# Optimization experiments

Hardware: AMD Instinct MI355X
Metric: run time of the kernel (lower is better)

The kernel has to match this reference:

```python
import jax, jax.numpy as jnp
import numpy as np


def setup_inputs() -> dict:
    key = jax.random.key(0)
    k1, k2, k3, k4 = jax.random.split(key, 4)
    B, T, D, H = 4, 4096, 1024, 64
    x = jax.random.normal(k1, (B, T, D), dtype=jnp.float32)
    # nn.Linear(n_embd, head_size, bias=False): store as [D, H] so x @ W matches
    scale = 1.0 / np.sqrt(D)
    Wq = jax.random.normal(k2, (D, H), dtype=jnp.float32) * scale
    Wk = jax.random.normal(k3, (D, H), dtype=jnp.float32) * scale
    Wv = jax.random.normal(k4, (D, H), dtype=jnp.float32) * scale
    return {"x": x, "Wq": Wq, "Wk": Wk, "Wv": Wv}


def reference(x, Wq, Wk, Wv):
    B, T, D = x.shape
    q = jnp.einsum('btd,dh->bth', x, Wq)
    k = jnp.einsum('btd,dh->bth', x, Wk)
    v = jnp.einsum('btd,dh->bth', x, Wv)
    # NOTE: original scales by D**-0.5 where D = n_embd (input dim), not head_size
    scores = jnp.einsum('bth,bsh->bts', q, k) * (D ** -0.5)  # [B,T,T]
    causal = jnp.tril(jnp.ones((T, T), dtype=bool))
    scores = jnp.where(causal, scores, -jnp.inf)
    attn = jax.nn.softmax(scores, axis=-1)
    return jnp.einsum('bts,bsh->bth', attn, v)
```

## Files before the change

kernel.cpp:

```cpp
#include <hip/hip_runtime.h>
#include <hip/hip_bf16.h>
#include <math.h>

typedef __attribute__((ext_vector_type(8))) short bf16x8;
typedef __attribute__((ext_vector_type(4))) float f32x4;
typedef __attribute__((ext_vector_type(16))) float f32x16;
typedef __attribute__((ext_vector_type(2))) unsigned uint2v;

#define MFMA16(A, B, C) __builtin_amdgcn_mfma_f32_16x16x32_bf16(A, B, C, 0, 0, 0)
#define MFMA32(A, B, C) __builtin_amdgcn_mfma_f32_32x32x16_bf16(A, B, C, 0, 0, 0)
#define LOG2E 1.44269504f
#define MB 5.7707801f

__device__ __forceinline__ short f2bf(float f) {
  union { __hip_bfloat16 b; short s; } v;
  v.b = __float2bfloat16(f);
  return v.s;
}

__device__ __forceinline__ float bf2f(short s) {
  union { unsigned u; float f; } v;
  v.u = ((unsigned)(unsigned short)s) << 16;
  return v.f;
}

__device__ __forceinline__ bf16x8 cvt8(float4 a, float4 b) {
  bf16x8 r;
  r[0] = f2bf(a.x); r[1] = f2bf(a.y); r[2] = f2bf(a.z); r[3] = f2bf(a.w);
  r[4] = f2bf(b.x); r[5] = f2bf(b.y); r[6] = f2bf(b.z); r[7] = f2bf(b.w);
  return r;
}

__device__ __forceinline__ unsigned cvt_pk(float lo, float hi) {
  unsigned r;
  asm("v_cvt_pk_bf16_f32 %0, %1, %2" : "=v"(r) : "v"(lo), "v"(hi));
  return r;
}

__device__ __forceinline__ void glds16(const void* g, void* l) {
  __builtin_amdgcn_global_load_lds(
      (const __attribute__((address_space(1))) unsigned int*)g,
      (__attribute__((address_space(3))) unsigned int*)l, 16, 0, 0);
}

__device__ __forceinline__ float xhalf_sum(float x) {
  uint2v r = __builtin_amdgcn_permlane32_swap(__float_as_uint(x), __float_as_uint(x),
                                              false, false);
  return __uint_as_float(r[0]) + __uint_as_float(r[1]);
}

__global__ __launch_bounds__(256) void prep_w(const float* __restrict__ Wq,
                                              const float* __restrict__ Wk,
                                              const float* __restrict__ Wv,
                                              short* __restrict__ Wt) {
  __shared__ float ls[64][65];
  const int wsel = blockIdx.x >> 4;
  const int dt = blockIdx.x & 15;
  const float* W = (wsel == 0) ? Wq : ((wsel == 1) ? Wk : Wv);
  const float scale = (wsel == 0) ? (0.03125f * LOG2E) : 1.0f;
  const int d0 = dt * 64;
  const int rr = threadIdx.x >> 4;
  const int cc = threadIdx.x & 15;
#pragma unroll
  for (int p = 0; p < 4; ++p) {
    int d = rr + p * 16;
    float4 v = *(const float4*)(W + (size_t)(d0 + d) * 64 + cc * 4);
    ls[d][cc * 4 + 0] = v.x; ls[d][cc * 4 + 1] = v.y;
    ls[d][cc * 4 + 2] = v.z; ls[d][cc * 4 + 3] = v.w;
  }
  __syncthreads();
#pragma unroll
  for (int p = 0; p < 4; ++p) {
    int h = rr + p * 16;
    short4 o;
    o.x = f2bf(ls[cc * 4 + 0][h] * scale);
    o.y = f2bf(ls[cc * 4 + 1][h] * scale);
    o.z = f2bf(ls[cc * 4 + 2][h] * scale);
    o.w = f2bf(ls[cc * 4 + 3][h] * scale);
    *(short4*)(Wt + (size_t)(wsel * 64 + h) * 1024 + d0 + cc * 4) = o;
  }
}

__global__ __launch_bounds__(256, 2) void qkv_kernel(const float* __restrict__ x,
                                                     const short* __restrict__ Wt,
                                                     short* __restrict__ qo,
                                                     short* __restrict__ ko,
                                                     short* __restrict__ vT) {
  __shared__ __align__(16) char pool[65536];
  const int tid = threadIdx.x;
  const int wave = tid >> 6, lane = tid & 63;
  const int lr = lane & 15, lq = lane >> 4;
  const int m0 = blockIdx.x * 32;

  f32x4 acc[2][3];
#pragma unroll
  for (int mi = 0; mi < 2; ++mi)
#pragma unroll
    for (int j = 0; j < 3; ++j) acc[mi][j] = f32x4{0.f, 0.f, 0.f, 0.f};

  const int xrow0 = wave * 4 + (lane >> 4);
  const int col16 = lane & 15;
  const float* xg[2];
#pragma unroll
  for (int r = 0; r < 2; ++r) {
    int row = xrow0 + r * 16;
    xg[r] = x + (size_t)(m0 + row) * 1024 + ((col16 ^ (row & 7)) << 2);
  }
  const int wswz = ((lane & 7) ^ (lane >> 3)) << 3;
  const short* wg[6];
#pragma unroll
  for (int r = 0; r < 6; ++r) {
    int n = wave * 8 + (lane >> 3) + r * 32;
    wg[r] = Wt + (size_t)n * 1024 + wswz;
  }
  const int xdst = wave * 1024;
  const int wdst = 8192 + wave * 1024;

#define STAGEQ(c, t)                                                        \
  {                                                                         \
    char* pb = pool + (c) * 32768;                                          \
    glds16(xg[0] + (t) * 64, pb + xdst);                                    \
    glds16(xg[1] + (t) * 64, pb + xdst + 4096);                             \
    _Pragma("unroll") for (int r = 0; r < 6; ++r)                           \
        glds16(wg[r] + (t) * 64, pb + wdst + r * 4096);                     \
  }

  STAGEQ(0, 0)
  __syncthreads();

  int cur = 0;
  for (int t = 0; t < 16; ++t) {
    if (t < 15) STAGEQ(cur ^ 1, t + 1)
    const char* xb = pool + cur * 32768;
    const char* wb = xb + 8192;
#pragma unroll
    for (int kc = 0; kc < 2; ++kc) {
      bf16x8 bfg[3];
#pragma unroll
      for (int j = 0; j < 3; ++j) {
        int n = (wave * 3 + j) * 16 + lr;
        int unit = kc * 4 + lq;
        bfg[j] = *(const bf16x8*)(wb + n * 128 + ((unit ^ (n & 7)) << 4));
      }
#pragma unroll
      for (int mi = 0; mi < 2; ++mi) {
        int row = mi * 16 + lr;
        int p = kc * 4 + lq;
        const char* xr = xb + row * 256;
        float4 a0 = *(const float4*)(xr + (((2 * p) ^ (row & 7)) << 4));
        float4 a1 = *(const float4*)(xr + (((2 * p + 1) ^ (row & 7)) << 4));
        bf16x8 af = cvt8(a0, a1);
#pragma unroll
        for (int j = 0; j < 3; ++j) acc[mi][j] = MFMA16(af, bfg[j], acc[mi][j]);
      }
    }
    __syncthreads();
    cur ^= 1;
  }
#undef STAGEQ

  short* els = (short*)pool;
#pragma unroll
  for (int j = 0; j < 3; ++j) {
    int nt = wave * 3 + j;
#pragma unroll
    for (int mi = 0; mi < 2; ++mi) {
      if (nt < 8) {
#pragma unroll
        for (int r = 0; r < 4; ++r) {
          int mloc = mi * 16 + lq * 4 + r;
          els[mloc * 136 + nt * 16 + lr] = f2bf(acc[mi][j][r]);
        }
      } else {
        int m = m0 + mi * 16 + lq * 4;
        short4 h;
        h.x = f2bf(acc[mi][j][0]); h.y = f2bf(acc[mi][j][1]);
        h.z = f2bf(acc[mi][j][2]); h.w = f2bf(acc[mi][j][3]);
        *(short4*)(vT + ((m >> 12) << 18) + ((nt * 16 + lr - 128) << 12) +
                   (m & 4095)) = h;
      }
    }
  }
  __syncthreads();
  {
    const int m = tid >> 3, nq = tid & 7;
    bf16x8 vq = *(const bf16x8*)(els + m * 136 + nq * 8);
    bf16x8 vk = *(const bf16x8*)(els + m * 136 + 64 + nq * 8);
    *(bf16x8*)(qo + (size_t)(m0 + m) * 64 + nq * 8) = vq;
    *(bf16x8*)(ko + (size_t)(m0 + m) * 64 + nq * 8) = vk;
  }
}

__global__ __launch_bounds__(256) void attn_partial(const short* __restrict__ qbuf,
                                                    const short* __restrict__ kbuf,
                                                    const short* __restrict__ vbuf,
                                                    short* __restrict__ Op,
                                                    float* __restrict__ lp) {
  __shared__ __align__(16) char kv_lds[2][16384];
  const int id = blockIdx.x;
  const int b = id & 3;
  const int u = id >> 2;
  int qt = 0, base = 0;
  while (u >= base + (qt >> 1) + 1) { base += (qt >> 1) + 1; ++qt; }
  const int seg = u - base;
  const int kv_lo = seg << 8;
  const int kv_hi = (seg == (qt >> 1)) ? (qt * 128 + 128) : ((seg + 1) << 8);

  const int tid = threadIdx.x;
  const int wv = tid >> 6, lane = tid & 63;
  const int l31 = lane & 31, hi = lane >> 5;
  const int qr0 = qt * 128 + wv * 32;
  const int qglob = qr0 + l31;

  const short* qb = qbuf + ((size_t)b << 18);
  const short* kb = kbuf + ((size_t)b << 18);
  const short* vb = vbuf + ((size_t)b << 18);

  bf16x8 bq[4];
#pragma unroll
  for (int c = 0; c < 4; ++c)
    bq[c] = *(const bf16x8*)(qb + (size_t)(qr0 + l31) * 64 + c * 16 + hi * 8);

  const int sr = (wv << 4) + (lane >> 3);
  const int swz_s = ((lane & 7) ^ (lane >> 3)) << 3;
  const short* ksrc = kb + (size_t)sr * 64 + swz_s;
  const short* vsrc = vb + (size_t)sr * 4096 + swz_s;
  const int kdst = (wv * 2) * 1024;
  const int vdst = 8192 + (wv * 2) * 1024;

#define STAGE(c, KV0)                                                       \
  {                                                                         \
    char* base_ = kv_lds[c];                                                \
    glds16(ksrc + (size_t)(KV0) * 64, base_ + kdst);                        \
    glds16(ksrc + (size_t)((KV0) + 8) * 64, base_ + kdst + 1024);           \
    glds16(vsrc + (KV0), base_ + vdst);                                     \
    glds16(vsrc + 8 * 4096 + (KV0), base_ + vdst + 1024);                   \
  }

  f32x16 o0, o1;
#pragma unroll
  for (int r = 0; r < 16; ++r) { o0[r] = 0.f; o1[r] = 0.f; }
  float lrow = 0.f;

  union U8 { unsigned u[4]; bf16x8 v; };
  const int swz_r = (l31 & 7);

  STAGE(0, kv_lo)
  __syncthreads();

  int cur = 0;
  for (int kv0 = kv_lo; kv0 < kv_hi; kv0 += 64) {
    if (kv0 + 64 < kv_hi) STAGE(cur ^ 1, kv0 + 64)

    if (kv0 <= qr0 + 31) {
      const int kv1 = kv0 + 32;
      const char* kl = kv_lds[cur];
      const char* vl = kv_lds[cur] + 8192;
      bf16x8 ka[4], kc[4], va[8];
#pragma unroll
      for (int c = 0; c < 4; ++c) {
        ka[c] = *(const bf16x8*)(kl + l31 * 128 + (((c * 2 + hi) ^ swz_r) << 4));
        kc[c] = *(const bf16x8*)(kl + (32 + l31) * 128 + (((c * 2 + hi) ^ swz_r) << 4));
      }
#pragma unroll
      for (int h = 0; h < 2; ++h)
#pragma unroll
        for (int p = 0; p < 4; ++p)
          va[h * 4 + p] = *(const bf16x8*)(vl + (32 * h + l31) * 128 +
                                           (((2 * p + hi) ^ swz_r) << 4));

      f32x16 s0, s1;
#pragma unroll
      for (int r = 0; r < 16; ++r) { s0[r] = 0.f; s1[r] = 0.f; }
#pragma unroll
      for (int c = 0; c < 4; ++c) {
        s0 = MFMA32(ka[c], bq[c], s0);
        s1 = MFMA32(kc[c], bq[c], s1);
      }

      if (kv0 + 31 > qr0) {
#pragma unroll
        for (int r = 0; r < 16; ++r)
          if (kv0 + (r & 3) + 8 * (r >> 2) + 4 * hi > qglob) s0[r] = -1e30f;
      }
      if (kv1 + 31 > qr0) {
#pragma unroll
        for (int r = 0; r < 16; ++r)
          if (kv1 + (r & 3) + 8 * (r >> 2) + 4 * hi > qglob) s1[r] = -1e30f;
      }

      float p0[16], p1[16];
#pragma unroll
      for (int r = 0; r < 16; ++r) {
        p0[r] = exp2f(s0[r] - MB);
        p1[r] = exp2f(s1[r] - MB);
      }
      float a8[8];
#pragma unroll
      for (int r = 0; r < 8; ++r) a8[r] = (p0[r] + p0[r + 8]) + (p1[r] + p1[r + 8]);
      float s4 = ((a8[0] + a8[4]) + (a8[1] + a8[5])) +
                 ((a8[2] + a8[6]) + (a8[3] + a8[7]));
      lrow += xhalf_sum(s4);

#define MAKE_FRAGS(P, UA, UB)                                                  \
      {                                                                        \
        unsigned c0 = cvt_pk(P[0], P[1]), c1 = cvt_pk(P[2], P[3]);             \
        unsigned c2 = cvt_pk(P[4], P[5]), c3 = cvt_pk(P[6], P[7]);             \
        unsigned c4 = cvt_pk(P[8], P[9]), c5 = cvt_pk(P[10], P[11]);           \
        unsigned c6 = cvt_pk(P[12], P[13]), c7 = cvt_pk(P[14], P[15]);         \
        uint2v rA = __builtin_amdgcn_permlane32_swap(c0, c2, false, false);    \
        uint2v rB = __builtin_amdgcn_permlane32_swap(c1, c3, false, false);    \
        uint2v rC = __builtin_amdgcn_permlane32_swap(c4, c6, false, false);    \
        uint2v rD = __builtin_amdgcn_permlane32_swap(c5, c7, false, false);    \
        UA.u[0] = rA[0]; UA.u[2] = rA[1];                                      \
        UA.u[1] = rB[0]; UA.u[3] = rB[1];                                      \
        UB.u[0] = rC[0]; UB.u[2] = rC[1];                                      \
        UB.u[1] = rD[0]; UB.u[3] = rD[1];                                      \
      }
      U8 pa00, pa01, pa10, pa11;
      MAKE_FRAGS(p0, pa00, pa01)
      MAKE_FRAGS(p1, pa10, pa11)
#undef MAKE_FRAGS

      o0 = MFMA32(va[0], pa00.v, o0);
      o0 = MFMA32(va[1], pa01.v, o0);
      o0 = MFMA32(va[2], pa10.v, o0);
      o0 = MFMA32(va[3], pa11.v, o0);
      o1 = MFMA32(va[4], pa00.v, o1);
      o1 = MFMA32(va[5], pa01.v, o1);
      o1 = MFMA32(va[6], pa10.v, o1);
      o1 = MFMA32(va[7], pa11.v, o1);
    }

    __syncthreads();
    cur ^= 1;
  }
#undef STAGE

  const int pid = b * 272 + u;
  short* Ob = Op + (size_t)pid * 8192;
#pragma unroll
  for (int r = 0; r < 16; ++r) {
    int hd = (r & 3) + 8 * (r >> 2) + 4 * hi;
    Ob[hd * 128 + wv * 32 + l31] = f2bf(o0[r]);
    Ob[(32 + hd) * 128 + wv * 32 + l31] = f2bf(o1[r]);
  }
  if (hi == 0) lp[pid * 128 + wv * 32 + l31] = lrow;
}

__global__ __launch_bounds__(256) void attn_combine(const short* __restrict__ Op,
                                                    const float* __restrict__ lp,
                                                    float* __restrict__ out) {
  __shared__ float ls[32][128];
  const int qt = blockIdx.x;
  const int b = blockIdx.y;
  const int zh = blockIdx.z;
  const int m = qt >> 1, e = qt & 1;
  const int nseg = m + 1;
  const int base = b * 272 + qt + m * (m - 1) + e * m;

  const int qc = threadIdx.x & 127, hh = threadIdx.x >> 7;
  float lsum = 0.f;
  for (int s = 0; s < nseg; ++s) lsum += lp[(base + s) * 128 + qc];
  const float inv = 1.0f / lsum;

  float osum[16];
#pragma unroll
  for (int i = 0; i < 16; ++i) osum[i] = 0.f;
  for (int s = 0; s < nseg; ++s) {
    const short* Ob = Op + (size_t)(base + s) * 8192;
#pragma unroll
    for (int i = 0; i < 16; ++i)
      osum[i] += bf2f(Ob[(zh * 32 + hh * 16 + i) * 128 + qc]);
  }
#pragma unroll
  for (int i = 0; i < 16; ++i) ls[hh * 16 + i][qc] = osum[i] * inv;
  __syncthreads();

  const int row = threadIdx.x >> 1, ch = (threadIdx.x & 1) * 16;
  float4 w4[4];
#pragma unroll
  for (int g4 = 0; g4 < 4; ++g4) {
    w4[g4].x = ls[ch + g4 * 4 + 0][row];
    w4[g4].y = ls[ch + g4 * 4 + 1][row];
    w4[g4].z = ls[ch + g4 * 4 + 2][row];
    w4[g4].w = ls[ch + g4 * 4 + 3][row];
  }
  float* op = out + ((size_t)b * 4096 + (size_t)qt * 128 + row) * 64 + zh * 32 + ch;
#pragma unroll
  for (int g4 = 0; g4 < 4; ++g4) *(float4*)(op + g4 * 4) = w4[g4];
}

extern "C" void kernel_launch(void* const* d_in, const int* in_sizes, int n_in,
                              void* d_out, int out_size, void* d_ws, size_t ws_size,
                              hipStream_t stream) {
  const float* x = (const float*)d_in[0];
  const float* Wq = (const float*)d_in[1];
  const float* Wk = (const float*)d_in[2];
  const float* Wv = (const float*)d_in[3];
  float* out = (float*)d_out;

  char* w = (char*)d_ws;
  short* qb = (short*)(w);
  short* kb = (short*)(w + (size_t)2 * 1024 * 1024);
  short* vT = (short*)(w + (size_t)4 * 1024 * 1024);
  short* Wt = (short*)(w + (size_t)6 * 1024 * 1024);
  float* lp = (float*)(w + (size_t)6656 * 1024);
  short* Op = (short*)(w + (size_t)7424 * 1024);

  prep_w<<<48, 256, 0, stream>>>(Wq, Wk, Wv, Wt);
  qkv_kernel<<<512, 256, 0, stream>>>(x, Wt, qb, kb, vT);
  attn_partial<<<1088, 256, 0, stream>>>(qb, kb, vT, Op, lp);
  attn_combine<<<dim3(32, 4, 2), 256, 0, stream>>>(Op, lp, out);
}
```

Measured before the change: 68.66 us.

## Shrink QKV projection tile to 16 rows and load weights directly into registers

The QKV projection kernel now handles 16 rows per block instead of 32 and launches twice as many blocks. Weight fragments are read straight from global memory into registers with double buffering, so only the x tile is staged in LDS. LDS use drops from 64KB to 8KB and the launch bound is raised to 4 blocks per CU. The goal is more parallelism and occupancy for a memory-bound projection, at the cost of each block re-reading the full weight matrix, which doubles total weight traffic (served mostly from cache).

Result: slower. 96.74 us (+40.9%).

```diff
diff --git a/kernel.cpp b/kernel.cpp
--- a/kernel.cpp
+++ b/kernel.cpp
@@ -81,113 +81,99 @@
   }
 }
 
-__global__ __launch_bounds__(256, 2) void qkv_kernel(const float* __restrict__ x,
+__global__ __launch_bounds__(256, 4) void qkv_kernel(const float* __restrict__ x,
                                                      const short* __restrict__ Wt,
                                                      short* __restrict__ qo,
                                                      short* __restrict__ ko,
                                                      short* __restrict__ vT) {
-  __shared__ __align__(16) char pool[65536];
+  __shared__ __align__(16) char pool[8192];
   const int tid = threadIdx.x;
   const int wave = tid >> 6, lane = tid & 63;
   const int lr = lane & 15, lq = lane >> 4;
-  const int m0 = blockIdx.x * 32;
-
-  f32x4 acc[2][3];
-#pragma unroll
-  for (int mi = 0; mi < 2; ++mi)
-#pragma unroll
-    for (int j = 0; j < 3; ++j) acc[mi][j] = f32x4{0.f, 0.f, 0.f, 0.f};
-
-  const int xrow0 = wave * 4 + (lane >> 4);
-  const int col16 = lane & 15;
-  const float* xg[2];
-#pragma unroll
-  for (int r = 0; r < 2; ++r) {
-    int row = xrow0 + r * 16;
-    xg[r] = x + (size_t)(m0 + row) * 1024 + ((col16 ^ (row & 7)) << 2);
-  }
-  const int wswz = ((lane & 7) ^ (lane >> 3)) << 3;
-  const short* wg[6];
-#pragma unroll
-  for (int r = 0; r < 6; ++r) {
-    int n = wave * 8 + (lane >> 3) + r * 32;
-    wg[r] = Wt + (size_t)n * 1024 + wswz;
-  }
+  const int m0 = blockIdx.x * 16;
+
+  f32x4 acc[3];
+#pragma unroll
+  for (int j = 0; j < 3; ++j) acc[j] = f32x4{0.f, 0.f, 0.f, 0.f};
+
+  const int srow = wave * 4 + (lane >> 4);
+  const float* xg = x + (size_t)(m0 + srow) * 1024 +
+                    (((lane & 15) ^ (srow & 7)) << 2);
   const int xdst = wave * 1024;
-  const int wdst = 8192 + wave * 1024;
-
-#define STAGEQ(c, t)                                                        \
+
+  const short* wg[3];
+#pragma unroll
+  for (int j = 0; j < 3; ++j)
+    wg[j] = Wt + (size_t)((wave * 3 + j) * 16 + lr) * 1024 + lq * 8;
+
+#define LOADW(W, t)                                                         \
+  _Pragma("unroll") for (int j = 0; j < 3; ++j)                             \
+  _Pragma("unroll") for (int kc = 0; kc < 2; ++kc)                          \
+      W[j * 2 + kc] = *(const bf16x8*)(wg[j] + (t) * 64 + kc * 32);
+
+#define QCOMP(XB, W)                                                        \
   {                                                                         \
-    char* pb = pool + (c) * 32768;                                          \
-    glds16(xg[0] + (t) * 64, pb + xdst);                                    \
-    glds16(xg[1] + (t) * 64, pb + xdst + 4096);                             \
-    _Pragma("unroll") for (int r = 0; r < 6; ++r)                           \
-        glds16(wg[r] + (t) * 64, pb + wdst + r * 4096);                     \
-  }
-
-  STAGEQ(0, 0)
+    const char* xb = (XB);                                                  \
+    _Pragma("unroll") for (int kc = 0; kc < 2; ++kc) {                      \
+      const int u0 = kc * 8 + lq * 2;                                       \
+      const char* xr = xb + lr * 256;                                       \
+      float4 a0 = *(const float4*)(xr + ((u0 ^ (lr & 7)) << 4));            \
+      float4 a1 = *(const float4*)(xr + (((u0 + 1) ^ (lr & 7)) << 4));      \
+      bf16x8 af = cvt8(a0, a1);                                             \
+      _Pragma("unroll") for (int j = 0; j < 3; ++j)                         \
+          acc[j] = MFMA16(af, W[j * 2 + kc], acc[j]);                       \
+    }                                                                       \
+  }
+
+  bf16x8 wA[6], wB[6];
+  glds16(xg, pool + xdst);
+  LOADW(wA, 0)
   __syncthreads();
 
-  int cur = 0;
-  for (int t = 0; t < 16; ++t) {
-    if (t < 15) STAGEQ(cur ^ 1, t + 1)
-    const char* xb = pool + cur * 32768;
-    const char* wb = xb + 8192;
-#pragma unroll
-    for (int kc = 0; kc < 2; ++kc) {
-      bf16x8 bfg[3];
-#pragma unroll
-      for (int j = 0; j < 3; ++j) {
-        int n = (wave * 3 + j) * 16 + lr;
-        int unit = kc * 4 + lq;
-        bfg[j] = *(const bf16x8*)(wb + n * 128 + ((unit ^ (n & 7)) << 4));
-      }
-#pragma unroll
-      for (int mi = 0; mi < 2; ++mi) {
-        int row = mi * 16 + lr;
-        int p = kc * 4 + lq;
-        const char* xr = xb + row * 256;
-        float4 a0 = *(const float4*)(xr + (((2 * p) ^ (row & 7)) << 4));
-        float4 a1 = *(const float4*)(xr + (((2 * p + 1) ^ (row & 7)) << 4));
-        bf16x8 af = cvt8(a0, a1);
-#pragma unroll
-        for (int j = 0; j < 3; ++j) acc[mi][j] = MFMA16(af, bfg[j], acc[mi][j]);
-      }
+  for (int t = 0; t < 16; t += 2) {
+    glds16(xg + (t + 1) * 64, pool + 4096 + xdst);
+    LOADW(wB, t + 1)
+    QCOMP(pool, wA)
+    __syncthreads();
+    if (t + 2 < 16) {
+      glds16(xg + (t + 2) * 64, pool + xdst);
+      LOADW(wA, t + 2)
     }
+    QCOMP(pool + 4096, wB)
     __syncthreads();
-    cur ^= 1;
-  }
-#undef STAGEQ
+  }
+#undef LOADW
+#undef QCOMP
 
   short* els = (short*)pool;
 #pragma unroll
   for (int j = 0; j < 3; ++j) {
     int nt = wave * 3 + j;
-#pragma unroll
-    for (int mi = 0; mi < 2; ++mi) {
-      if (nt < 8) {
-#pragma unroll
-        for (int r = 0; r < 4; ++r) {
-          int mloc = mi * 16 + lq * 4 + r;
-          els[mloc * 136 + nt * 16 + lr] = f2bf(acc[mi][j][r]);
-        }
-      } else {
-        int m = m0 + mi * 16 + lq * 4;
-        short4 h;
-        h.x = f2bf(acc[mi][j][0]); h.y = f2bf(acc[mi][j][1]);
-        h.z = f2bf(acc[mi][j][2]); h.w = f2bf(acc[mi][j][3]);
-        *(short4*)(vT + ((m >> 12) << 18) + ((nt * 16 + lr - 128) << 12) +
-                   (m & 4095)) = h;
-      }
+    if (nt < 8) {
+#pragma unroll
+      for (int r = 0; r < 4; ++r) {
+        int mloc = lq * 4 + r;
+        els[mloc * 136 + nt * 16 + lr] = f2bf(acc[j][r]);
+      }
+    } else {
+      int m = m0 + lq * 4;
+      short4 h;
+      h.x = f2bf(acc[j][0]); h.y = f2bf(acc[j][1]);
+      h.z = f2bf(acc[j][2]); h.w = f2bf(acc[j][3]);
+      *(short4*)(vT + ((m >> 12) << 18) + ((nt * 16 + lr - 128) << 12) +
+                 (m & 4095)) = h;
     }
   }
   __syncthreads();
   {
-    const int m = tid >> 3, nq = tid & 7;
-    bf16x8 vq = *(const bf16x8*)(els + m * 136 + nq * 8);
-    bf16x8 vk = *(const bf16x8*)(els + m * 136 + 64 + nq * 8);
-    *(bf16x8*)(qo + (size_t)(m0 + m) * 64 + nq * 8) = vq;
-    *(bf16x8*)(ko + (size_t)(m0 + m) * 64 + nq * 8) = vk;
+    const int m = tid >> 4, c = tid & 15;
+    if (c < 8) {
+      bf16x8 vq = *(const bf16x8*)(els + m * 136 + c * 8);
+      *(bf16x8*)(qo + (size_t)(m0 + m) * 64 + c * 8) = vq;
+    } else {
+      bf16x8 vk = *(const bf16x8*)(els + m * 136 + 64 + (c - 8) * 8);
+      *(bf16x8*)(ko + (size_t)(m0 + m) * 64 + (c - 8) * 8) = vk;
+    }
   }
 }
 
@@ -409,7 +395,7 @@
   short* Op = (short*)(w + (size_t)7424 * 1024);
 
   prep_w<<<48, 256, 0, stream>>>(Wq, Wk, Wv, Wt);
-  qkv_kernel<<<512, 256, 0, stream>>>(x, Wt, qb, kb, vT);
+  qkv_kernel<<<1024, 256, 0, stream>>>(x, Wt, qb, kb, vT);
   attn_partial<<<1088, 256, 0, stream>>>(qb, kb, vT, Op, lp);
   attn_combine<<<dim3(32, 4, 2), 256, 0, stream>>>(Op, lp, out);
 }
```
